# Performance work log

Measured on AMD Instinct MI355X. Metric: run time of the kernel, lower is better.

The kernel has to match this reference:

```python
import jax, jax.numpy as jnp
import numpy as np

N, IN_DIM, NUM_HEADS, HEAD_DIM = 8192, 256, 4, 64
NEG_SLOPE = 0.2


def setup_inputs() -> dict:
    key = jax.random.key(0)
    k1, k2, k3, k4 = jax.random.split(key, 4)
    h = jax.random.normal(k1, (N, IN_DIM), dtype=jnp.float32)
    adj = jax.random.randint(k2, (N, N), 0, 2, dtype=jnp.int32)
    # xavier-ish init scale for the per-head projection weights and attention vector
    W = jax.random.normal(k3, (NUM_HEADS, IN_DIM, HEAD_DIM), dtype=jnp.float32) * (1.0 / np.sqrt(IN_DIM))
    a = jax.random.normal(k4, (2 * HEAD_DIM, 1), dtype=jnp.float32) * (1.0 / np.sqrt(2 * HEAD_DIM))
    return {"h": h, "adj": adj, "W": W, "a": a}


def reference(h, adj, W, a):
    # Wh: (H, N, D) -- per-head linear projection (no bias)
    Wh = jnp.einsum('ni,hid->hnd', h, W)
    # torch computes cat([Wh_i, Wh_j]) @ a; equivalent decomposition:
    # e_ij = (Wh_i . a[:D]) + (Wh_j . a[D:])  -- avoids the O(N^2 * 2D) concat tensor
    a1 = a[:HEAD_DIM, 0]  # (D,)
    a2 = a[HEAD_DIM:, 0]  # (D,)
    s_i = jnp.einsum('hnd,d->hn', Wh, a1)  # (H, N)
    s_j = jnp.einsum('hnd,d->hn', Wh, a2)  # (H, N)
    e = s_i[:, :, None] + s_j[:, None, :]  # (H, N, N)
    e = jnp.where(e > 0, e, NEG_SLOPE * e)  # leaky_relu(0.2)
    e = jnp.where(adj[None, :, :] == 0, -jnp.inf, e)
    att = jax.nn.softmax(e, axis=-1)  # torch softmax(dim=1) over last axis of (N,N)
    # dropout is identity in eval mode
    out = jnp.einsum('hnm,hmd->hnd', att, Wh)  # (H, N, D)
    # concat head outputs along feature dim -> (N, H*D)
    return jnp.transpose(out, (1, 0, 2)).reshape(N, NUM_HEADS * HEAD_DIM)
```

## Files before the change

kernel.cpp:

```cpp
#include <hip/hip_runtime.h>
#include <hip/hip_bf16.h>

#define NND 8192
#define NHEADS 4
#define HD 64

typedef __attribute__((ext_vector_type(8))) __bf16 bf16x8;
typedef __attribute__((ext_vector_type(4))) float f32x4;
typedef __attribute__((ext_vector_type(4))) unsigned int u32x4;
typedef __attribute__((ext_vector_type(4))) int i32x4;

__global__ __launch_bounds__(256) void gat_phase1(
    const float* __restrict__ hin, const float* __restrict__ W, const float* __restrict__ av,
    float* __restrict__ s1, float* __restrict__ s2, unsigned short* __restrict__ whbT)
{
  __shared__ __align__(16) float hl[32][256];
  const int t = threadIdx.x;
  const int n0 = blockIdx.x * 32;
  #pragma unroll
  for (int k = 0; k < 8; ++k) {
    int off = k * 1024 + t * 4;
    int r = off >> 8, c = off & 255;
    *(f32x4*)&hl[r][c] = *(const f32x4*)&hin[(size_t)(n0 + r) * 256 + c];
  }
  __syncthreads();
  const int head = t >> 6;
  const int d = t & 63;
  const int lane = t & 63;
  const float* Wc = W + head * 256 * 64 + d;
  float acc[32];
  #pragma unroll
  for (int n = 0; n < 32; ++n) acc[n] = 0.f;
  for (int i0 = 0; i0 < 256; i0 += 4) {
    float w0 = Wc[(i0 + 0) * 64];
    float w1 = Wc[(i0 + 1) * 64];
    float w2 = Wc[(i0 + 2) * 64];
    float w3 = Wc[(i0 + 3) * 64];
    #pragma unroll
    for (int n = 0; n < 32; ++n) {
      f32x4 hv = *(const f32x4*)&hl[n][i0];
      float a0 = __builtin_fmaf(hv[0], w0, acc[n]);
      float a1 = __builtin_fmaf(hv[1], w1, a0);
      float a2 = __builtin_fmaf(hv[2], w2, a1);
      acc[n]   = __builtin_fmaf(hv[3], w3, a2);
    }
  }
  const float a1v = av[d];
  const float a2v = av[64 + d];
  #pragma unroll
  for (int n = 0; n < 32; ++n) {
    float v1 = acc[n] * a1v;
    float v2 = acc[n] * a2v;
    #pragma unroll
    for (int off = 32; off; off >>= 1) {
      v1 += __shfl_xor(v1, off, 64);
      v2 += __shfl_xor(v2, off, 64);
    }
    if (lane == 0) {
      s1[head * NND + n0 + n] = v1;
      s2[head * NND + n0 + n] = v2;
    }
  }
  #pragma unroll
  for (int k = 0; k < 4; ++k) {
    union { unsigned short us[8]; u32x4 v; } u;
    #pragma unroll
    for (int e = 0; e < 8; ++e)
      u.us[e] = __builtin_bit_cast(unsigned short, (__bf16)acc[k * 8 + e]);
    *(u32x4*)&whbT[(size_t)t * NND + n0 + k * 8] = u.v;
  }
}

__global__ __launch_bounds__(512) void gat_phase2(
    const int* __restrict__ adj, const float* __restrict__ s1, const float* __restrict__ s2,
    const unsigned short* __restrict__ whbT, float* __restrict__ out)
{
  __shared__ __align__(16) int adjT[32 * 68];
  const int t = threadIdx.x;
  const int wave = t >> 6, lane = t & 63;
  const int head = wave & 3, rhalf = wave >> 2;
  const int i0 = blockIdx.x * 32;
  const int lo = lane & 15, kg = lane >> 4;
  const int rowA = rhalf * 16 + lo;
  const float s1v = s1[head * NND + i0 + rowA];
  const float* s2h = s2 + head * NND;
  const unsigned short* wb = whbT + (size_t)(head * 64 + lo) * NND;
  f32x4 acc[4];
  #pragma unroll
  for (int dt = 0; dt < 4; ++dt) acc[dt] = (f32x4)(0.f);
  float denom = 0.f;
  const int stR = t >> 4, stC = (t & 15) * 4;
  const int* adjP = adj + (size_t)(i0 + stR) * NND + stC;

  for (int jt = 0; jt < 128; ++jt) {
    const int j0 = jt * 64;
    i32x4 st = *(const i32x4*)(adjP + j0);
    bf16x8 bfr[8];
    #pragma unroll
    for (int ks = 0; ks < 2; ++ks) {
      #pragma unroll
      for (int dt = 0; dt < 4; ++dt) {
        bfr[ks * 4 + dt] = __builtin_bit_cast(bf16x8,
            *(const u32x4*)(wb + (size_t)dt * 16 * NND + j0 + ks * 32 + kg * 8));
      }
    }
    f32x4 sA = *(const f32x4*)&s2h[j0 + kg * 8];
    f32x4 sB = *(const f32x4*)&s2h[j0 + kg * 8 + 4];
    f32x4 sC = *(const f32x4*)&s2h[j0 + 32 + kg * 8];
    f32x4 sD = *(const f32x4*)&s2h[j0 + 32 + kg * 8 + 4];
    __syncthreads();
    *(i32x4*)&adjT[stR * 68 + stC] = st;
    __syncthreads();
    #pragma unroll
    for (int ks = 0; ks < 2; ++ks) {
      const int jb = ks * 32 + kg * 8;
      i32x4 m0 = *(const i32x4*)&adjT[rowA * 68 + jb];
      i32x4 m1 = *(const i32x4*)&adjT[rowA * 68 + jb + 4];
      f32x4 sx = ks ? sC : sA;
      f32x4 sy = ks ? sD : sB;
      bf16x8 af;
      float ds = 0.f;
      #pragma unroll
      for (int e = 0; e < 4; ++e) {
        float x = s1v + sx[e];
        x = fmaxf(x, 0.2f * x);
        x = (m0[e] != 0) ? x : -1e30f;
        float w = __expf(x);
        __bf16 wv = (__bf16)w;
        af[e] = wv;
        ds += (float)wv;
      }
      #pragma unroll
      for (int e = 0; e < 4; ++e) {
        float x = s1v + sy[e];
        x = fmaxf(x, 0.2f * x);
        x = (m1[e] != 0) ? x : -1e30f;
        float w = __expf(x);
        __bf16 wv = (__bf16)w;
        af[4 + e] = wv;
        ds += (float)wv;
      }
      denom += ds;
      #pragma unroll
      for (int dt = 0; dt < 4; ++dt)
        acc[dt] = __builtin_amdgcn_mfma_f32_16x16x32_bf16(af, bfr[ks * 4 + dt], acc[dt], 0, 0, 0);
    }
  }
  denom += __shfl_xor(denom, 16, 64);
  denom += __shfl_xor(denom, 32, 64);
  float rrec[4];
  #pragma unroll
  for (int r = 0; r < 4; ++r) {
    float dr = __shfl(denom, kg * 4 + r, 64);
    rrec[r] = 1.0f / dr;
  }
  float* op = out + (size_t)(i0 + rhalf * 16 + kg * 4) * 256 + head * 64 + lo;
  #pragma unroll
  for (int dt = 0; dt < 4; ++dt) {
    #pragma unroll
    for (int r = 0; r < 4; ++r)
      op[r * 256 + dt * 16] = acc[dt][r] * rrec[r];
  }
}

extern "C" void kernel_launch(void* const* d_in, const int* in_sizes, int n_in,
                              void* d_out, int out_size, void* d_ws, size_t ws_size,
                              hipStream_t stream) {
  const float* h   = (const float*)d_in[0];
  const int*   adj = (const int*)d_in[1];
  const float* W   = (const float*)d_in[2];
  const float* a   = (const float*)d_in[3];
  float* out = (float*)d_out;
  float* s1 = (float*)d_ws;
  float* s2 = s1 + NHEADS * NND;
  unsigned short* whbT = (unsigned short*)(s2 + NHEADS * NND);
  gat_phase1<<<dim3(NND / 32), dim3(256), 0, stream>>>(h, W, a, s1, s2, whbT);
  gat_phase2<<<dim3(NND / 32), dim3(512), 0, stream>>>(adj, s1, s2, whbT, out);
}
```

Baseline: 648.7 us.

## Use MFMA for projection and split-K attention across waves with LDS reduction

Phase 1 now computes the per-head projection with bf16 MFMA over 16-row tiles instead of scalar FMAs from an LDS-staged tile. Phase 2 uses 1024-thread blocks in which each wave handles two 16-row groups for one head and one quarter of the neighbour range. The partial accumulators and denominators are then reduced through shared memory. Adjacency is read directly from global memory instead of being staged through LDS, and masked entries now produce exactly zero weight. This removes the per-tile barriers and reuses each B fragment for two row groups, at the cost of a serial LDS reduction and higher register pressure.

Result: faster. 568.0 us (-12.4%).

```diff
diff --git a/kernel.cpp b/kernel.cpp
--- a/kernel.cpp
+++ b/kernel.cpp
@@ -2,8 +2,6 @@
 #include <hip/hip_bf16.h>
 
 #define NND 8192
-#define NHEADS 4
-#define HD 64
 
 typedef __attribute__((ext_vector_type(8))) __bf16 bf16x8;
 typedef __attribute__((ext_vector_type(4))) float f32x4;
@@ -14,152 +12,187 @@
     const float* __restrict__ hin, const float* __restrict__ W, const float* __restrict__ av,
     float* __restrict__ s1, float* __restrict__ s2, unsigned short* __restrict__ whbT)
 {
-  __shared__ __align__(16) float hl[32][256];
   const int t = threadIdx.x;
-  const int n0 = blockIdx.x * 32;
-  #pragma unroll
-  for (int k = 0; k < 8; ++k) {
-    int off = k * 1024 + t * 4;
-    int r = off >> 8, c = off & 255;
-    *(f32x4*)&hl[r][c] = *(const f32x4*)&hin[(size_t)(n0 + r) * 256 + c];
-  }
-  __syncthreads();
-  const int head = t >> 6;
-  const int d = t & 63;
-  const int lane = t & 63;
-  const float* Wc = W + head * 256 * 64 + d;
-  float acc[32];
-  #pragma unroll
-  for (int n = 0; n < 32; ++n) acc[n] = 0.f;
-  for (int i0 = 0; i0 < 256; i0 += 4) {
-    float w0 = Wc[(i0 + 0) * 64];
-    float w1 = Wc[(i0 + 1) * 64];
-    float w2 = Wc[(i0 + 2) * 64];
-    float w3 = Wc[(i0 + 3) * 64];
-    #pragma unroll
-    for (int n = 0; n < 32; ++n) {
-      f32x4 hv = *(const f32x4*)&hl[n][i0];
-      float a0 = __builtin_fmaf(hv[0], w0, acc[n]);
-      float a1 = __builtin_fmaf(hv[1], w1, a0);
-      float a2 = __builtin_fmaf(hv[2], w2, a1);
-      acc[n]   = __builtin_fmaf(hv[3], w3, a2);
-    }
-  }
-  const float a1v = av[d];
-  const float a2v = av[64 + d];
-  #pragma unroll
-  for (int n = 0; n < 32; ++n) {
-    float v1 = acc[n] * a1v;
-    float v2 = acc[n] * a2v;
-    #pragma unroll
-    for (int off = 32; off; off >>= 1) {
-      v1 += __shfl_xor(v1, off, 64);
-      v2 += __shfl_xor(v2, off, 64);
-    }
-    if (lane == 0) {
-      s1[head * NND + n0 + n] = v1;
-      s2[head * NND + n0 + n] = v2;
-    }
-  }
-  #pragma unroll
-  for (int k = 0; k < 4; ++k) {
-    union { unsigned short us[8]; u32x4 v; } u;
-    #pragma unroll
-    for (int e = 0; e < 8; ++e)
-      u.us[e] = __builtin_bit_cast(unsigned short, (__bf16)acc[k * 8 + e]);
-    *(u32x4*)&whbT[(size_t)t * NND + n0 + k * 8] = u.v;
+  const int head = t >> 6, lane = t & 63;
+  const int lo = lane & 15, kg = lane >> 4;
+  const int n0 = blockIdx.x * 16;
+  const float* hrow = hin + (size_t)(n0 + lo) * 256;
+  const float* Wp = W + head * 16384;
+  f32x4 acc[4];
+  #pragma unroll
+  for (int rt = 0; rt < 4; ++rt) acc[rt] = (f32x4)(0.f);
+
+  #pragma unroll 2
+  for (int ks = 0; ks < 8; ++ks) {
+    const int kb = ks * 32 + kg * 8;
+    f32x4 h0 = *(const f32x4*)(hrow + kb);
+    f32x4 h1 = *(const f32x4*)(hrow + kb + 4);
+    bf16x8 bf;
+    #pragma unroll
+    for (int e = 0; e < 4; ++e) { bf[e] = (__bf16)h0[e]; bf[e + 4] = (__bf16)h1[e]; }
+    #pragma unroll
+    for (int rt = 0; rt < 4; ++rt) {
+      bf16x8 af;
+      #pragma unroll
+      for (int e = 0; e < 8; ++e)
+        af[e] = (__bf16)Wp[(kb + e) * 64 + rt * 16 + lo];
+      acc[rt] = __builtin_amdgcn_mfma_f32_16x16x32_bf16(af, bf, acc[rt], 0, 0, 0);
+    }
+  }
+  #pragma unroll
+  for (int rt = 0; rt < 4; ++rt) {
+    #pragma unroll
+    for (int r = 0; r < 4; ++r) {
+      int hd = head * 64 + rt * 16 + kg * 4 + r;
+      whbT[(size_t)hd * NND + n0 + lo] =
+          __builtin_bit_cast(unsigned short, (__bf16)acc[rt][r]);
+    }
+  }
+  float p1 = 0.f, p2 = 0.f;
+  #pragma unroll
+  for (int rt = 0; rt < 4; ++rt) {
+    #pragma unroll
+    for (int r = 0; r < 4; ++r) {
+      int d = rt * 16 + kg * 4 + r;
+      p1 = __builtin_fmaf(acc[rt][r], av[d], p1);
+      p2 = __builtin_fmaf(acc[rt][r], av[64 + d], p2);
+    }
+  }
+  p1 += __shfl_xor(p1, 16, 64); p1 += __shfl_xor(p1, 32, 64);
+  p2 += __shfl_xor(p2, 16, 64); p2 += __shfl_xor(p2, 32, 64);
+  if (kg == 0) {
+    s1[head * NND + n0 + lo] = p1;
+    s2[head * NND + n0 + lo] = p2;
   }
 }
 
-__global__ __launch_bounds__(512) void gat_phase2(
+__global__ __launch_bounds__(1024, 4) void gat_phase2(
     const int* __restrict__ adj, const float* __restrict__ s1, const float* __restrict__ s2,
     const unsigned short* __restrict__ whbT, float* __restrict__ out)
 {
-  __shared__ __align__(16) int adjT[32 * 68];
+  __shared__ float red[4][64][36];
   const int t = threadIdx.x;
   const int wave = t >> 6, lane = t & 63;
-  const int head = wave & 3, rhalf = wave >> 2;
+  const int head = wave & 3, jseg = wave >> 2;
   const int i0 = blockIdx.x * 32;
   const int lo = lane & 15, kg = lane >> 4;
-  const int rowA = rhalf * 16 + lo;
-  const float s1v = s1[head * NND + i0 + rowA];
+  const float s1v0 = s1[head * NND + i0 + lo];
+  const float s1v1 = s1[head * NND + i0 + 16 + lo];
   const float* s2h = s2 + head * NND;
-  const unsigned short* wb = whbT + (size_t)(head * 64 + lo) * NND;
-  f32x4 acc[4];
-  #pragma unroll
-  for (int dt = 0; dt < 4; ++dt) acc[dt] = (f32x4)(0.f);
-  float denom = 0.f;
-  const int stR = t >> 4, stC = (t & 15) * 4;
-  const int* adjP = adj + (size_t)(i0 + stR) * NND + stC;
-
-  for (int jt = 0; jt < 128; ++jt) {
-    const int j0 = jt * 64;
-    i32x4 st = *(const i32x4*)(adjP + j0);
-    bf16x8 bfr[8];
+  const unsigned short* wb0 = whbT + (size_t)(head * 64 + lo) * NND;
+  const unsigned short* wb1 = wb0 + (size_t)16 * NND;
+  const unsigned short* wb2 = wb0 + (size_t)32 * NND;
+  const unsigned short* wb3 = wb0 + (size_t)48 * NND;
+  const int* adjR0 = adj + (size_t)(i0 + lo) * NND;
+  const int* adjR1 = adj + (size_t)(i0 + 16 + lo) * NND;
+  f32x4 acc0[4], acc1[4];
+  #pragma unroll
+  for (int dt = 0; dt < 4; ++dt) { acc0[dt] = (f32x4)(0.f); acc1[dt] = (f32x4)(0.f); }
+  float den0 = 0.f, den1 = 0.f;
+  const int jbase = jseg * 2048;
+
+  for (int jt = 0; jt < 32; ++jt) {
+    const int j0 = jbase + jt * 64;
     #pragma unroll
     for (int ks = 0; ks < 2; ++ks) {
+      const int jb = j0 + ks * 32 + kg * 8;
+      u32x4 b0 = *(const u32x4*)(wb0 + jb);
+      u32x4 b1 = *(const u32x4*)(wb1 + jb);
+      u32x4 b2 = *(const u32x4*)(wb2 + jb);
+      u32x4 b3 = *(const u32x4*)(wb3 + jb);
+      i32x4 m0a = *(const i32x4*)(adjR0 + jb);
+      i32x4 m0b = *(const i32x4*)(adjR0 + jb + 4);
+      i32x4 m1a = *(const i32x4*)(adjR1 + jb);
+      i32x4 m1b = *(const i32x4*)(adjR1 + jb + 4);
+      f32x4 sa = *(const f32x4*)(s2h + jb);
+      f32x4 sb = *(const f32x4*)(s2h + jb + 4);
+      {
+        bf16x8 af;
+        #pragma unroll
+        for (int e = 0; e < 4; ++e) {
+          float x = s1v0 + sa[e];
+          x = fmaxf(x, 0.2f * x);
+          float w = (m0a[e] != 0) ? __expf(x) : 0.0f;
+          af[e] = (__bf16)w;
+          den0 += (float)af[e];
+        }
+        #pragma unroll
+        for (int e = 0; e < 4; ++e) {
+          float x = s1v0 + sb[e];
+          x = fmaxf(x, 0.2f * x);
+          float w = (m0b[e] != 0) ? __expf(x) : 0.0f;
+          af[e + 4] = (__bf16)w;
+          den0 += (float)af[e + 4];
+        }
+        acc0[0] = __builtin_amdgcn_mfma_f32_16x16x32_bf16(af, __builtin_bit_cast(bf16x8, b0), acc0[0], 0, 0, 0);
+        acc0[1] = __builtin_amdgcn_mfma_f32_16x16x32_bf16(af, __builtin_bit_cast(bf16x8, b1), acc0[1], 0, 0, 0);
+        acc0[2] = __builtin_amdgcn_mfma_f32_16x16x32_bf16(af, __builtin_bit_cast(bf16x8, b2), acc0[2], 0, 0, 0);
+        acc0[3] = __builtin_amdgcn_mfma_f32_16x16x32_bf16(af, __builtin_bit_cast(bf16x8, b3), acc0[3], 0, 0, 0);
+      }
+      {
+        bf16x8 af;
+        #pragma unroll
+        for (int e = 0; e < 4; ++e) {
+          float x = s1v1 + sa[e];
+          x = fmaxf(x, 0.2f * x);
+          float w = (m1a[e] != 0) ? __expf(x) : 0.0f;
+          af[e] = (__bf16)w;
+          den1 += (float)af[e];
+        }
+        #pragma unroll
+        for (int e = 0; e < 4; ++e) {
+          float x = s1v1 + sb[e];
+          x = fmaxf(x, 0.2f * x);
+          float w = (m1b[e] != 0) ? __expf(x) : 0.0f;
+          af[e + 4] = (__bf16)w;
+          den1 += (float)af[e + 4];
+        }
+        acc1[0] = __builtin_amdgcn_mfma_f32_16x16x32_bf16(af, __builtin_bit_cast(bf16x8, b0), acc1[0], 0, 0, 0);
+        acc1[1] = __builtin_amdgcn_mfma_f32_16x16x32_bf16(af, __builtin_bit_cast(bf16x8, b1), acc1[1], 0, 0, 0);
+        acc1[2] = __builtin_amdgcn_mfma_f32_16x16x32_bf16(af, __builtin_bit_cast(bf16x8, b2), acc1[2], 0, 0, 0);
+        acc1[3] = __builtin_amdgcn_mfma_f32_16x16x32_bf16(af, __builtin_bit_cast(bf16x8, b3), acc1[3], 0, 0, 0);
+      }
+    }
+  }
+  den0 += __shfl_xor(den0, 16, 64); den0 += __shfl_xor(den0, 32, 64);
+  den1 += __shfl_xor(den1, 16, 64); den1 += __shfl_xor(den1, 32, 64);
+
+  for (int s = 1; s <= 3; ++s) {
+    if (jseg == s) {
       #pragma unroll
       for (int dt = 0; dt < 4; ++dt) {
-        bfr[ks * 4 + dt] = __builtin_bit_cast(bf16x8,
-            *(const u32x4*)(wb + (size_t)dt * 16 * NND + j0 + ks * 32 + kg * 8));
-      }
-    }
-    f32x4 sA = *(const f32x4*)&s2h[j0 + kg * 8];
-    f32x4 sB = *(const f32x4*)&s2h[j0 + kg * 8 + 4];
-    f32x4 sC = *(const f32x4*)&s2h[j0 + 32 + kg * 8];
-    f32x4 sD = *(const f32x4*)&s2h[j0 + 32 + kg * 8 + 4];
+        *(f32x4*)&red[head][lane][dt * 4]      = acc0[dt];
+        *(f32x4*)&red[head][lane][16 + dt * 4] = acc1[dt];
+      }
+      red[head][lane][32] = den0;
+      red[head][lane][33] = den1;
+    }
     __syncthreads();
-    *(i32x4*)&adjT[stR * 68 + stC] = st;
+    if (jseg == 0) {
+      #pragma unroll
+      for (int dt = 0; dt < 4; ++dt) {
+        acc0[dt] += *(const f32x4*)&red[head][lane][dt * 4];
+        acc1[dt] += *(const f32x4*)&red[head][lane][16 + dt * 4];
+      }
+      den0 += red[head][lane][32];
+      den1 += red[head][lane][33];
+    }
     __syncthreads();
-    #pragma unroll
-    for (int ks = 0; ks < 2; ++ks) {
-      const int jb = ks * 32 + kg * 8;
-      i32x4 m0 = *(const i32x4*)&adjT[rowA * 68 + jb];
-      i32x4 m1 = *(const i32x4*)&adjT[rowA * 68 + jb + 4];
-      f32x4 sx = ks ? sC : sA;
-      f32x4 sy = ks ? sD : sB;
-      bf16x8 af;
-      float ds = 0.f;
-      #pragma unroll
-      for (int e = 0; e < 4; ++e) {
-        float x = s1v + sx[e];
-        x = fmaxf(x, 0.2f * x);
-        x = (m0[e] != 0) ? x : -1e30f;
-        float w = __expf(x);
-        __bf16 wv = (__bf16)w;
-        af[e] = wv;
-        ds += (float)wv;
-      }
-      #pragma unroll
-      for (int e = 0; e < 4; ++e) {
-        float x = s1v + sy[e];
-        x = fmaxf(x, 0.2f * x);
-        x = (m1[e] != 0) ? x : -1e30f;
-        float w = __expf(x);
-        __bf16 wv = (__bf16)w;
-        af[4 + e] = wv;
-        ds += (float)wv;
-      }
-      denom += ds;
-      #pragma unroll
-      for (int dt = 0; dt < 4; ++dt)
-        acc[dt] = __builtin_amdgcn_mfma_f32_16x16x32_bf16(af, bfr[ks * 4 + dt], acc[dt], 0, 0, 0);
-    }
-  }
-  denom += __shfl_xor(denom, 16, 64);
-  denom += __shfl_xor(denom, 32, 64);
-  float rrec[4];
+  }
+  if (jseg != 0) return;
+
   #pragma unroll
   for (int r = 0; r < 4; ++r) {
-    float dr = __shfl(denom, kg * 4 + r, 64);
-    rrec[r] = 1.0f / dr;
-  }
-  float* op = out + (size_t)(i0 + rhalf * 16 + kg * 4) * 256 + head * 64 + lo;
-  #pragma unroll
-  for (int dt = 0; dt < 4; ++dt) {
-    #pragma unroll
-    for (int r = 0; r < 4; ++r)
-      op[r * 256 + dt * 16] = acc[dt][r] * rrec[r];
+    float dr0 = __shfl(den0, kg * 4 + r, 64);
+    float dr1 = __shfl(den1, kg * 4 + r, 64);
+    float rc0 = 1.0f / dr0, rc1 = 1.0f / dr1;
+    float* op0 = out + (size_t)(i0 + kg * 4 + r) * 256 + head * 64 + lo;
+    float* op1 = out + (size_t)(i0 + 16 + kg * 4 + r) * 256 + head * 64 + lo;
+    #pragma unroll
+    for (int dt = 0; dt < 4; ++dt) {
+      op0[dt * 16] = acc0[dt][r] * rc0;
+      op1[dt * 16] = acc1[dt][r] * rc1;
+    }
   }
 }
 
@@ -172,8 +205,8 @@
   const float* a   = (const float*)d_in[3];
   float* out = (float*)d_out;
   float* s1 = (float*)d_ws;
-  float* s2 = s1 + NHEADS * NND;
-  unsigned short* whbT = (unsigned short*)(s2 + NHEADS * NND);
-  gat_phase1<<<dim3(NND / 32), dim3(256), 0, stream>>>(h, W, a, s1, s2, whbT);
-  gat_phase2<<<dim3(NND / 32), dim3(512), 0, stream>>>(adj, s1, s2, whbT, out);
+  float* s2 = s1 + 4 * NND;
+  unsigned short* whbT = (unsigned short*)(s2 + 4 * NND);
+  gat_phase1<<<dim3(NND / 16), dim3(256), 0, stream>>>(h, W, a, s1, s2, whbT);
+  gat_phase2<<<dim3(NND / 32), dim3(1024), 0, stream>>>(adj, s1, s2, whbT, out);
 }
```
